# Optimization experiments

Measured on AMD Instinct MI355X. Metric: run time of the kernel, lower is better.

The kernel has to match this reference:

```python
import jax, jax.numpy as jnp
import numpy as np

B, S, H, I, E, TOP_K = 1, 2048, 1024, 4096, 8, 1


def setup_inputs() -> dict:
    key = jax.random.key(0)
    ks = jax.random.split(key, 8)
    s = 0.02  # init scale for weights
    return {
        "hidden_states": jax.random.normal(ks[0], (B, S, H), jnp.float32),
        "router_w": jax.random.normal(ks[1], (E, H), jnp.float32) * s,
        "w_gate": jax.random.normal(ks[2], (E, I, H), jnp.float32) * s,
        "w_up": jax.random.normal(ks[3], (E, I, H), jnp.float32) * s,
        "w_down": jax.random.normal(ks[4], (E, H, I), jnp.float32) * s,
        "ws_gate": jax.random.normal(ks[5], (I, H), jnp.float32) * s,
        "ws_up": jax.random.normal(ks[6], (I, H), jnp.float32) * s,
        "ws_down": jax.random.normal(ks[7], (H, I), jnp.float32) * s,
    }


def _mlp(x, wg, wu, wd):
    # silu(x @ Wg^T) * (x @ Wu^T) @ Wd^T  (Llama4TextMLP)
    return (jax.nn.silu(x @ wg.T) * (x @ wu.T)) @ wd.T


def reference(hidden_states, router_w, w_gate, w_up, w_down, ws_gate, ws_up, ws_down):
    b, s, h = hidden_states.shape
    hs = hidden_states.reshape(-1, h)                      # [T, H]
    T = hs.shape[0]
    logits = hs @ router_w.T                               # [T, E]
    top_v, top_i = jax.lax.top_k(logits, TOP_K)            # [T, K]
    masked = jnp.full_like(logits, -jnp.inf)
    masked = masked.at[jnp.arange(T)[:, None], top_i].set(top_v)
    scores = jax.nn.sigmoid(masked)                        # [T, E]; sigmoid(-inf)=0

    # In this module every expert sees ALL tokens, scaled by its (mostly-zero) score.
    routed = scores.T[:, :, None] * hs[None, :, :]         # [E, T, H]

    out = _mlp(hs, ws_gate, ws_up, ws_down)                # shared expert, [T, H]
    gate = jnp.einsum('eth,eih->eti', routed, w_gate)      # [E, T, I]
    up = jnp.einsum('eth,eih->eti', routed, w_up)          # [E, T, I]
    expert_out = jnp.einsum('eti,ehi->eth', jax.nn.silu(gate) * up, w_down)
    out = out + expert_out.sum(axis=0)                     # [T, H]
    return out, scores.T                                   # router_scores is [E, T]
```

## Files before the change

kernel.cpp:

```cpp
#include <hip/hip_runtime.h>
#include <hip/hip_bf16.h>
#include <math.h>

#define T_TOK 2048
#define HDIM 1024
#define IDIM 4096
#define NEXP 8
#define RROWS 3200
#define AROWS 5248
#define ZROW  5120
#define NP2   24
#define BK 32

typedef unsigned int uint;
typedef unsigned short ushort;
typedef __attribute__((ext_vector_type(4))) float f32x4;
typedef __attribute__((ext_vector_type(8))) short bf16x8;

__device__ __forceinline__ ushort f2bf(float f) {
  union { float f; uint u; } c; c.f = f;
  uint u = c.u;
  return (ushort)((u + 0x7FFFu + ((u >> 16) & 1u)) >> 16);
}
__device__ __forceinline__ uint cvtpk(float a, float b) {
  uint r;
  asm("v_cvt_pk_bf16_f32 %0, %1, %2" : "=v"(r) : "v"(a), "v"(b));
  return r;
}
__device__ __forceinline__ uint4 cvt8(const float4 a, const float4 b) {
  uint4 r;
  r.x = cvtpk(a.x, a.y); r.y = cvtpk(a.z, a.w);
  r.z = cvtpk(b.x, b.y); r.w = cvtpk(b.z, b.w);
  return r;
}
__device__ __forceinline__ void gld16(ushort* lds, const ushort* g) {
  __builtin_amdgcn_global_load_lds(
      (const __attribute__((address_space(1))) uint*)g,
      (__attribute__((address_space(3))) uint*)lds, 16, 0, 0);
}
__device__ __forceinline__ int soff(int row, int kc) {
  return ((row >> 4) << 9) + (kc << 7) + ((row & 15) << 3);
}

#define SYNCV(N) { \
  __builtin_amdgcn_sched_barrier(0); \
  asm volatile("s_waitcnt vmcnt(" #N ") lgkmcnt(0)" ::: "memory"); \
  __builtin_amdgcn_s_barrier(); \
  __builtin_amdgcn_sched_barrier(0); }

__global__ __launch_bounds__(256) void router_kernel(
    const float* __restrict__ hs, const float* __restrict__ rw,
    ushort* __restrict__ Xall, float* __restrict__ scores_out,
    int* __restrict__ eidx, float* __restrict__ sval)
{
  const int wave = threadIdx.x >> 6;
  const int lane = threadIdx.x & 63;
  const int t = blockIdx.x * 4 + wave;
  const float* row = hs + (size_t)t * HDIM;
  float v[16];
  #pragma unroll
  for (int i = 0; i < 16; ++i) {
    v[i] = row[lane + 64 * i];
    Xall[(size_t)t * HDIM + lane + 64 * i] = f2bf(v[i]);
  }
  float logit[8];
  #pragma unroll
  for (int e = 0; e < 8; ++e) {
    const float* wr = rw + e * HDIM;
    float s = 0.f;
    #pragma unroll
    for (int i = 0; i < 16; ++i) s += v[i] * wr[lane + 64 * i];
    #pragma unroll
    for (int off = 32; off; off >>= 1) s += __shfl_xor(s, off, 64);
    logit[e] = s;
  }
  if (lane == 0) {
    int be = 0; float bv = logit[0];
    #pragma unroll
    for (int e = 1; e < 8; ++e) if (logit[e] > bv) { bv = logit[e]; be = e; }
    float sc = 1.f / (1.f + expf(-bv));
    eidx[t] = be; sval[t] = sc;
    #pragma unroll
    for (int e = 0; e < 8; ++e) scores_out[(size_t)e * T_TOK + t] = (e == be) ? sc : 0.f;
  }
}

__global__ __launch_bounds__(256) void plan_kernel(
    const int* __restrict__ eidx, int* __restrict__ row2tok, int4* __restrict__ pairs)
{
  __shared__ int cnt[8];
  __shared__ int slot[8];
  const int tid = threadIdx.x;
  if (tid < 8) cnt[tid] = 0;
  __syncthreads();
  for (int t = tid; t < T_TOK; t += 256) atomicAdd(&cnt[eidx[t]], 1);
  __syncthreads();
  if (tid == 0) {
    int np = 0;
    for (int i = 0; i < 8; ++i) pairs[np++] = make_int4(i * 256, i * 256 + 128, -1, 1);
    int o = 0;
    for (int e = 0; e < 8; ++e) {
      slot[e] = o;
      int cap = (cnt[e] + 127) & ~127;
      int nt = cap / 128;
      for (int j = 0; j < nt; j += 2) {
        int ra = T_TOK + o + j * 128;
        int rb = (j + 1 < nt) ? ra + 128 : ZROW;
        pairs[np++] = make_int4(ra, rb, e, 1);
      }
      o += cap;
    }
    for (; np < NP2; ++np) pairs[np] = make_int4(ZROW, ZROW, 0, 0);
  }
  for (int r = tid; r < RROWS; r += 256) row2tok[r] = -1;
  __syncthreads();
  for (int t = tid; t < T_TOK; t += 256) {
    int e = eidx[t];
    int s = atomicAdd(&slot[e], 1);
    row2tok[s] = t;
  }
}

__global__ __launch_bounds__(256) void gather_kernel(
    const float* __restrict__ hs, const int* __restrict__ row2tok,
    const float* __restrict__ sval, ushort* __restrict__ Xall)
{
  const int r = blockIdx.x;
  const int t = row2tok[r];
  const int c0 = threadIdx.x * 4;
  ushort4 o;
  if (t >= 0) {
    const float sc = sval[t];
    float4 v = *(const float4*)(hs + (size_t)t * HDIM + c0);
    o.x = f2bf(sc * v.x); o.y = f2bf(sc * v.y); o.z = f2bf(sc * v.z); o.w = f2bf(sc * v.w);
  } else { o.x = o.y = o.z = o.w = 0; }
  *(ushort4*)(Xall + (size_t)(T_TOK + r) * HDIM + c0) = o;
}

#define LOADB1(S, k0) { \
  gr##S = *(const float4*)(gptr + (k0)); \
  ur##S = *(const float4*)(uptr + (k0)); }

#define WRITEB1(S, B) { \
  *(uint2*)&Bg[B][woff] = make_uint2(cvtpk(gr##S.x, gr##S.y), cvtpk(gr##S.z, gr##S.w)); \
  *(uint2*)&Bu[B][woff] = make_uint2(cvtpk(ur##S.x, ur##S.y), cvtpk(ur##S.z, ur##S.w)); }

#define STAGEA1(ABASE, k0) { gld16((ABASE) + alds0, asrc0 + (k0)); }

#define READ1(ABASE, B) \
  bf16x8 af[4], gf[2], uf[2]; \
  _Pragma("unroll") \
  for (int m = 0; m < 4; ++m) af[m] = *(const bf16x8*)((ABASE) + (wm*4+m)*512 + lp); \
  _Pragma("unroll") \
  for (int n = 0; n < 2; ++n) { \
    gf[n] = *(const bf16x8*)&Bg[B][(wn*2+n)*512 + lp]; \
    uf[n] = *(const bf16x8*)&Bu[B][(wn*2+n)*512 + lp]; }

#define MFMA1 \
  _Pragma("unroll") \
  for (int m = 0; m < 4; ++m) { \
    _Pragma("unroll") \
    for (int n = 0; n < 2; ++n) { \
      accg[m][n] = __builtin_amdgcn_mfma_f32_16x16x32_bf16(af[m], gf[n], accg[m][n], 0, 0, 0); \
      accu[m][n] = __builtin_amdgcn_mfma_f32_16x16x32_bf16(af[m], uf[n], accu[m][n], 0, 0, 0); } }

#define ROTA { ushort* aT_ = aR; aR = aM; aM = aS; aS = aT_; }

__global__ __launch_bounds__(1024, 1) void gemm1_kernel(
    const ushort* __restrict__ Xall,
    const float* __restrict__ w_gate, const float* __restrict__ w_up,
    const float* __restrict__ ws_gate, const float* __restrict__ ws_up,
    const int4* __restrict__ pairs, ushort* __restrict__ actall)
{
  __shared__ __align__(16) ushort As[3][8192];
  __shared__ __align__(16) ushort Bg[2][4096];
  __shared__ __align__(16) ushort Bu[2][4096];

  const int b0 = blockIdx.x;
  const int j = b0 & 7, s = b0 >> 3;
  const int panel = j + 8 * (s / NP2);
  const int4 td = pairs[s % NP2];
  if (td.w == 0) return;
  const int r0a = td.x, r0b = td.y, e = td.z;
  const float* __restrict__ gbase = (e < 0) ? ws_gate : w_gate + (size_t)e * IDIM * HDIM;
  const float* __restrict__ ubase = (e < 0) ? ws_up   : w_up   + (size_t)e * IDIM * HDIM;
  const int col0 = panel * 128;

  const int tid = threadIdx.x;
  const int lane = tid & 63;
  const int w = tid >> 6;
  const int wm = w >> 2, wn = w & 3;

  const int brow = tid >> 3, bch = tid & 7;
  const float* gptr = gbase + (size_t)(col0 + brow) * HDIM + bch * 4;
  const float* uptr = ubase + (size_t)(col0 + brow) * HDIM + bch * 4;
  const int woff = soff(brow, bch >> 1) + (bch & 1) * 4;

  const size_t abs0 = (w < 8) ? (size_t)(r0a + w * 16 + (lane & 15))
                              : (size_t)(r0b + (w - 8) * 16 + (lane & 15));
  const ushort* asrc0 = Xall + abs0 * HDIM + (lane >> 4) * 8;
  const int alds0 = w * 512 + lane * 8;

  ushort* aR = &As[0][0];
  ushort* aM = &As[1][0];
  ushort* aS = &As[2][0];

  float4 gr0, ur0, gr1, ur1;
  const int lp = (lane >> 4) * 128 + (lane & 15) * 8;
  f32x4 accg[4][2] = {};
  f32x4 accu[4][2] = {};

  STAGEA1(aR, 0);
  LOADB1(0, 0);
  STAGEA1(aM, BK);
  LOADB1(1, BK);
  WRITEB1(0, 0);
  SYNCV(3);

  const int NS = HDIM / BK;
  for (int kk = 0; kk < NS / 2 - 1; ++kk) {
    const int k = kk * 2;
    {
      READ1(aR, 0);
      STAGEA1(aS, (k + 2) * BK);
      LOADB1(0, (k + 2) * BK);
      WRITEB1(1, 1);
      MFMA1;
      SYNCV(3);
      ROTA;
    }
    {
      READ1(aR, 1);
      STAGEA1(aS, (k + 3) * BK);
      LOADB1(1, (k + 3) * BK);
      WRITEB1(0, 0);
      MFMA1;
      SYNCV(3);
      ROTA;
    }
  }
  {
    READ1(aR, 0);
    WRITEB1(1, 1);
    MFMA1;
    SYNCV(0);
    ROTA;
  }
  {
    READ1(aR, 1);
    MFMA1;
  }

  const int prbase = wm * 64 + ((lane >> 4) << 2);
  const int cbase = col0 + wn * 32 + (lane & 15);
  #pragma unroll
  for (int m = 0; m < 4; ++m)
    #pragma unroll
    for (int n = 0; n < 2; ++n)
      #pragma unroll
      for (int j2 = 0; j2 < 4; ++j2) {
        const int pr = prbase + m * 16 + j2;
        const size_t ar = (wm < 2) ? (size_t)(r0a + pr) : (size_t)(r0b + pr - 128);
        float g = accg[m][n][j2];
        float u = accu[m][n][j2];
        float sv = g / (1.f + __expf(-g)) * u;
        actall[ar * IDIM + cbase + n * 16] = f2bf(sv);
      }
}

#define LOADB2(S, k0) { \
  const float4* bp_ = (const float4*)(bptr + (k0)); \
  br##S[0] = bp_[0]; br##S[1] = bp_[1]; }

#define WRITEB2(S, B) { *(uint4*)&Bs[B][woff2] = cvt8(br##S[0], br##S[1]); }

#define STAGEA2(ABASE, k0) { \
  gld16((ABASE) + alds0, asrc0 + (k0)); \
  gld16((ABASE) + alds1, asrc1 + (k0)); }

#define READ2(ABASE, B) \
  bf16x8 af[4], bfr[4]; \
  _Pragma("unroll") \
  for (int m = 0; m < 4; ++m) af[m] = *(const bf16x8*)((ABASE) + (wm*4+m)*512 + lp); \
  _Pragma("unroll") \
  for (int n = 0; n < 4; ++n) bfr[n] = *(const bf16x8*)&Bs[B][(wn*4+n)*512 + lp];

#define MFMA2 \
  _Pragma("unroll") \
  for (int m = 0; m < 4; ++m) { \
    _Pragma("unroll") \
    for (int n = 0; n < 4; ++n) \
      acc[m][n] = __builtin_amdgcn_mfma_f32_16x16x32_bf16(af[m], bfr[n], acc[m][n], 0, 0, 0); }

__global__ __launch_bounds__(512, 1) void gemm2_kernel(
    const ushort* __restrict__ actall,
    const float* __restrict__ w_down, const float* __restrict__ ws_down,
    const int4* __restrict__ pairs, const int* __restrict__ row2tok,
    float* __restrict__ out, float* __restrict__ bufr)
{
  __shared__ __align__(16) ushort As[3][8192];
  __shared__ __align__(16) ushort Bs[2][4096];

  const int b0 = blockIdx.x;
  const int panel = b0 & 7;
  const int4 td = pairs[b0 >> 3];
  if (td.w == 0) return;
  const int r0a = td.x, r0b = td.y, e = td.z;
  const float* __restrict__ bbase = (e < 0) ? ws_down : w_down + (size_t)e * HDIM * IDIM;
  const int col0 = panel * 128;

  const int tid = threadIdx.x;
  const int lane = tid & 63;
  const int w = tid >> 6;
  const int wm = w >> 1, wn = w & 1;

  const int brow = tid >> 2, kcb = tid & 3;
  const float* bptr = bbase + (size_t)(col0 + brow) * IDIM + kcb * 8;
  const int woff2 = soff(brow, kcb);

  const int arow = w * 32 + (lane & 15);
  const size_t abs0 = (w < 4) ? (size_t)(r0a + arow) : (size_t)(r0b + arow - 128);
  const ushort* asrc0 = actall + abs0 * IDIM + (lane >> 4) * 8;
  const ushort* asrc1 = asrc0 + (size_t)16 * IDIM;
  const int alds0 = w * 1024 + lane * 8;
  const int alds1 = alds0 + 512;

  ushort* aR = &As[0][0];
  ushort* aM = &As[1][0];
  ushort* aS = &As[2][0];

  float4 br0[2], br1[2];
  const int lp = (lane >> 4) * 128 + (lane & 15) * 8;
  f32x4 acc[4][4] = {};

  STAGEA2(aR, 0);
  LOADB2(0, 0);
  STAGEA2(aM, BK);
  LOADB2(1, BK);
  WRITEB2(0, 0);
  SYNCV(4);

  const int NS = IDIM / BK;
  for (int kk = 0; kk < NS / 2 - 1; ++kk) {
    const int k = kk * 2;
    {
      READ2(aR, 0);
      STAGEA2(aS, (k + 2) * BK);
      LOADB2(0, (k + 2) * BK);
      WRITEB2(1, 1);
      MFMA2;
      SYNCV(4);
      ROTA;
    }
    {
      READ2(aR, 1);
      STAGEA2(aS, (k + 3) * BK);
      LOADB2(1, (k + 3) * BK);
      WRITEB2(0, 0);
      MFMA2;
      SYNCV(4);
      ROTA;
    }
  }
  {
    READ2(aR, 0);
    WRITEB2(1, 1);
    MFMA2;
    SYNCV(0);
    ROTA;
  }
  {
    READ2(aR, 1);
    MFMA2;
  }

  const int prbase = wm * 64 + ((lane >> 4) << 2);
  const int cbase = col0 + wn * 64 + (lane & 15);
  #pragma unroll
  for (int m = 0; m < 4; ++m)
    #pragma unroll
    for (int j2 = 0; j2 < 4; ++j2) {
      const int pr = prbase + m * 16 + j2;
      const int ar = (wm < 2) ? (r0a + pr) : (r0b + pr - 128);
      if (e < 0) {
        #pragma unroll
        for (int n = 0; n < 4; ++n)
          out[(size_t)ar * HDIM + cbase + n * 16] = acc[m][n][j2];
      } else {
        const int t = row2tok[ar - T_TOK];
        if (t >= 0) {
          #pragma unroll
          for (int n = 0; n < 4; ++n)
            bufr[(size_t)t * HDIM + cbase + n * 16] = acc[m][n][j2];
        }
      }
    }
}

__global__ __launch_bounds__(256) void add_kernel(
    float* __restrict__ out, const float* __restrict__ bufr)
{
  const size_t i = ((size_t)blockIdx.x * 256 + threadIdx.x) * 4;
  float4 a = *(float4*)(out + i);
  const float4 b = *(const float4*)(bufr + i);
  a.x += b.x; a.y += b.y; a.z += b.z; a.w += b.w;
  *(float4*)(out + i) = a;
}

extern "C" void kernel_launch(void* const* d_in, const int* in_sizes, int n_in,
                              void* d_out, int out_size, void* d_ws, size_t ws_size,
                              hipStream_t stream)
{
  const float* hs      = (const float*)d_in[0];
  const float* rw      = (const float*)d_in[1];
  const float* w_gate  = (const float*)d_in[2];
  const float* w_up    = (const float*)d_in[3];
  const float* w_down  = (const float*)d_in[4];
  const float* ws_gate = (const float*)d_in[5];
  const float* ws_up   = (const float*)d_in[6];
  const float* ws_down = (const float*)d_in[7];

  float* out = (float*)d_out;
  float* scores_out = out + (size_t)T_TOK * HDIM;

  char* ws = (char*)d_ws;
  ushort* Xall   = (ushort*)ws;
  ushort* actall = (ushort*)(ws + 10747904);
  float*  bufr   = (float*)(ws + 53739520);
  int*    eidx   = (int*)(ws + 62128128);
  float*  sval   = (float*)(ws + 62136320);
  int*    r2t    = (int*)(ws + 62144512);
  int4*   pairs  = (int4*)(ws + 62157312);

  router_kernel<<<T_TOK / 4, 256, 0, stream>>>(hs, rw, Xall, scores_out, eidx, sval);
  plan_kernel<<<1, 256, 0, stream>>>(eidx, r2t, pairs);
  gather_kernel<<<RROWS, 256, 0, stream>>>(hs, r2t, sval, Xall);
  gemm1_kernel<<<(IDIM / 128) * NP2, 1024, 0, stream>>>(
      Xall, w_gate, w_up, ws_gate, ws_up, pairs, actall);
  gemm2_kernel<<<(HDIM / 128) * NP2, 512, 0, stream>>>(
      actall, w_down, ws_down, pairs, r2t, out, bufr);
  add_kernel<<<(T_TOK * HDIM) / 1024, 256, 0, stream>>>(out, bufr);
}
```

Before: 329.4 us.

## Reorder MFMA before B writes and shrink gemm2 A staging to double buffer

In gemm1 the MFMA block now issues before the converted B tile is written to shared memory, so matrix math can overlap the LDS store. In gemm2 the A tile staging drops from a triple-buffered rotation to two fixed buffers. Each A tile is now loaded one step ahead instead of two, the vmcnt wait shrinks, and sched_barriers pin the order of the async loads. This cuts LDS use and pointer rotation but gives less time to hide global load latency for A.

```diff
diff --git a/kernel.cpp b/kernel.cpp
--- a/kernel.cpp
+++ b/kernel.cpp
@@ -224,8 +224,8 @@
       READ1(aR, 0);
       STAGEA1(aS, (k + 2) * BK);
       LOADB1(0, (k + 2) * BK);
+      MFMA1;
       WRITEB1(1, 1);
-      MFMA1;
       SYNCV(3);
       ROTA;
     }
@@ -233,16 +233,16 @@
       READ1(aR, 1);
       STAGEA1(aS, (k + 3) * BK);
       LOADB1(1, (k + 3) * BK);
+      MFMA1;
       WRITEB1(0, 0);
-      MFMA1;
       SYNCV(3);
       ROTA;
     }
   }
   {
     READ1(aR, 0);
+    MFMA1;
     WRITEB1(1, 1);
-    MFMA1;
     SYNCV(0);
     ROTA;
   }
@@ -274,14 +274,14 @@
 
 #define WRITEB2(S, B) { *(uint4*)&Bs[B][woff2] = cvt8(br##S[0], br##S[1]); }
 
-#define STAGEA2(ABASE, k0) { \
-  gld16((ABASE) + alds0, asrc0 + (k0)); \
-  gld16((ABASE) + alds1, asrc1 + (k0)); }
-
-#define READ2(ABASE, B) \
+#define STAGEA2(B, k0) { \
+  gld16(&As[B][alds0], asrc0 + (k0)); \
+  gld16(&As[B][alds1], asrc1 + (k0)); }
+
+#define READ2(B) \
   bf16x8 af[4], bfr[4]; \
   _Pragma("unroll") \
-  for (int m = 0; m < 4; ++m) af[m] = *(const bf16x8*)((ABASE) + (wm*4+m)*512 + lp); \
+  for (int m = 0; m < 4; ++m) af[m] = *(const bf16x8*)&As[B][(wm*4+m)*512 + lp]; \
   _Pragma("unroll") \
   for (int n = 0; n < 4; ++n) bfr[n] = *(const bf16x8*)&Bs[B][(wn*4+n)*512 + lp];
 
@@ -298,7 +298,7 @@
     const int4* __restrict__ pairs, const int* __restrict__ row2tok,
     float* __restrict__ out, float* __restrict__ bufr)
 {
-  __shared__ __align__(16) ushort As[3][8192];
+  __shared__ __align__(16) ushort As[2][8192];
   __shared__ __align__(16) ushort Bs[2][4096];
 
   const int b0 = blockIdx.x;
@@ -325,52 +325,49 @@
   const int alds0 = w * 1024 + lane * 8;
   const int alds1 = alds0 + 512;
 
-  ushort* aR = &As[0][0];
-  ushort* aM = &As[1][0];
-  ushort* aS = &As[2][0];
-
   float4 br0[2], br1[2];
   const int lp = (lane >> 4) * 128 + (lane & 15) * 8;
   f32x4 acc[4][4] = {};
 
-  STAGEA2(aR, 0);
+  STAGEA2(0, 0);
+  __builtin_amdgcn_sched_barrier(0);
   LOADB2(0, 0);
-  STAGEA2(aM, BK);
+  WRITEB2(0, 0);
   LOADB2(1, BK);
-  WRITEB2(0, 0);
-  SYNCV(4);
+  SYNCV(2);
 
   const int NS = IDIM / BK;
   for (int kk = 0; kk < NS / 2 - 1; ++kk) {
     const int k = kk * 2;
     {
-      READ2(aR, 0);
-      STAGEA2(aS, (k + 2) * BK);
+      READ2(0);
+      STAGEA2(1, (k + 1) * BK);
+      __builtin_amdgcn_sched_barrier(0);
+      WRITEB2(1, 1);
       LOADB2(0, (k + 2) * BK);
-      WRITEB2(1, 1);
       MFMA2;
-      SYNCV(4);
-      ROTA;
+      SYNCV(2);
     }
     {
-      READ2(aR, 1);
-      STAGEA2(aS, (k + 3) * BK);
+      READ2(1);
+      STAGEA2(0, (k + 2) * BK);
+      __builtin_amdgcn_sched_barrier(0);
+      WRITEB2(0, 0);
       LOADB2(1, (k + 3) * BK);
-      WRITEB2(0, 0);
       MFMA2;
-      SYNCV(4);
-      ROTA;
+      SYNCV(2);
     }
   }
   {
-    READ2(aR, 0);
+    READ2(0);
+    STAGEA2(1, (NS - 1) * BK);
+    __builtin_amdgcn_sched_barrier(0);
     WRITEB2(1, 1);
     MFMA2;
     SYNCV(0);
-    ROTA;
   }
   {
-    READ2(aR, 1);
+    READ2(1);
     MFMA2;
   }
 
```

After: 295.8 us, median of 2. 10.2% less time.
